# Kernel tuning notes

Hardware: AMD Instinct MI355X
Metric: run time of the kernel (lower is better)

Reference implementation:

```python
import jax, jax.numpy as jnp
import numpy as np

DIM = 4096
HEAD_DIM = 512
ROPE_DIM = 64
NOPE_DIM = HEAD_DIM - ROPE_DIM  # 448
RATIO = 4
COFF = 2  # overlap since ratio == 4
EPS = 1e-6
NEG = -1e30
COMPRESS_ROPE_THETA = 40000.0


def _hadamard(n):
    H = np.array([[1.0]], dtype=np.float32)
    while H.shape[0] < n:
        H = np.block([[H, H], [H, -H]])
    return (H / np.sqrt(n)).astype(np.float32)

H_MAT = jnp.asarray(_hadamard(HEAD_DIM))  # [512, 512], orthonormal Hadamard


def setup_inputs() -> dict:
    key = jax.random.key(0)
    ks = jax.random.split(key, 5)
    b, s = 4, 4096
    x = jax.random.normal(ks[0], (b, s, DIM), dtype=jnp.float32)
    W_kv = jax.random.normal(ks[1], (COFF * HEAD_DIM, DIM), dtype=jnp.float32) * 0.02
    W_gate = jax.random.normal(ks[2], (COFF * HEAD_DIM, DIM), dtype=jnp.float32) * 0.02
    ape = jax.random.normal(ks[3], (RATIO, COFF * HEAD_DIM), dtype=jnp.float32) * 0.02
    norm_w = jnp.ones((HEAD_DIM,), dtype=jnp.float32)
    # rotary table over compressed-block positions
    nb = s // RATIO
    inv_freq = 1.0 / (COMPRESS_ROPE_THETA ** (jnp.arange(0, ROPE_DIM, 2, dtype=jnp.float32) / ROPE_DIM))
    ang = jnp.arange(nb, dtype=jnp.float32)[:, None] * inv_freq[None, :]  # [nb, 32]
    freqs_cis = jnp.stack([jnp.cos(ang), jnp.sin(ang)], axis=-1)  # [nb, 32, 2]
    return {"x": x, "W_kv": W_kv, "W_gate": W_gate, "ape": ape,
            "norm_w": norm_w, "freqs_cis": freqs_cis, "start_pos": 0}


def _overlap_transform(t, fill):
    # t: [b, nb, RATIO, 2*d] -> [b, nb, 2*RATIO, d]
    b, nb, r, dd = t.shape
    d = dd // 2
    prev_first = jnp.concatenate(
        [jnp.full((b, 1, r, d), fill, t.dtype), t[:, :-1, :, :d]], axis=1)
    return jnp.concatenate([prev_first, t[..., d:]], axis=2)


def reference(x, W_kv, W_gate, ape, norm_w, freqs_cis, start_pos):
    b, s, _ = x.shape
    nb = s // RATIO
    # block-wise projections with absolute-within-block positional bias
    kv = jnp.einsum('bsd,od->bso', x, W_kv).reshape(b, nb, RATIO, COFF * HEAD_DIM) + ape
    score = jnp.einsum('bsd,od->bso', x, W_gate).reshape(b, nb, RATIO, COFF * HEAD_DIM)
    # overlap with previous block: [b, nb, 2*RATIO, HEAD_DIM]
    kv_w = _overlap_transform(kv, 0.0)
    sc_w = _overlap_transform(score, NEG)
    # channelwise softmax-gated pooling over the 2*RATIO window
    w = jax.nn.softmax(sc_w, axis=2)
    pooled = jnp.sum(w * kv_w, axis=2)  # [b, nb, HEAD_DIM]
    # RMSNorm
    var = jnp.mean(jnp.square(pooled), axis=-1, keepdims=True)
    pooled = norm_w * (pooled * jax.lax.rsqrt(var + EPS))
    # rotary on the rope slice
    nope, rope = pooled[..., :NOPE_DIM], pooled[..., NOPE_DIM:]
    rp = rope.reshape(b, nb, ROPE_DIM // 2, 2)
    xr, xi = rp[..., 0], rp[..., 1]
    fr, fi = freqs_cis[None, :, :, 0], freqs_cis[None, :, :, 1]
    rot = jnp.stack([xr * fr - xi * fi, xr * fi + xi * fr], axis=-1).reshape(b, nb, ROPE_DIM)
    out = jnp.concatenate([nope, rot], axis=-1)  # [b, nb, HEAD_DIM]
    # Hadamard rotation (rotate_activation)
    out = out @ H_MAT
    return out
```

## Files before the change

### kernel.cpp

```cpp
#include <hip/hip_runtime.h>
#include <hip/hip_bf16.h>
#include <stdint.h>

#define M_ROWS 16384
#define N_COLS 2048
#define K_DIM  4096
#define NEGV   -1e30f

typedef __bf16 bfv8 __attribute__((ext_vector_type(8)));
typedef float  f32x4 __attribute__((ext_vector_type(4)));
typedef unsigned short u16;

static __device__ __forceinline__ u16 f32_to_bf16_rne(float f) {
  union { float f; unsigned int u; } v; v.f = f;
  unsigned int u = v.u;
  u += 0x7fffu + ((u >> 16) & 1u);
  return (u16)(u >> 16);
}

static __device__ __forceinline__ float b2f(u16 b) {
  union { unsigned int u; float f; } v; v.u = ((unsigned int)b) << 16;
  return v.f;
}

__global__ __launch_bounds__(256) void k_cvt(const float* __restrict__ x,
                                             const float* __restrict__ wkv,
                                             const float* __restrict__ wg,
                                             u16* __restrict__ dst) {
  long i = (long)blockIdx.x * blockDim.x + threadIdx.x;
  long base = i * 8;
  const float* src;
  if (base < 67108864L) {
    src = x + base;
  } else {
    long wi = base - 67108864L;
    src = (wi < 4194304L) ? (wkv + wi) : (wg + (wi - 4194304L));
  }
  float4 a = *(const float4*)(src);
  float4 b = *(const float4*)(src + 4);
  union { u16 s[8]; uint4 v; } o;
  o.s[0] = f32_to_bf16_rne(a.x); o.s[1] = f32_to_bf16_rne(a.y);
  o.s[2] = f32_to_bf16_rne(a.z); o.s[3] = f32_to_bf16_rne(a.w);
  o.s[4] = f32_to_bf16_rne(b.x); o.s[5] = f32_to_bf16_rne(b.y);
  o.s[6] = f32_to_bf16_rne(b.z); o.s[7] = f32_to_bf16_rne(b.w);
  *(uint4*)(dst + base) = o.v;
}

#define GLD16(g, l) __builtin_amdgcn_global_load_lds( \
    (const __attribute__((address_space(1))) unsigned int*)(g), \
    (__attribute__((address_space(3))) unsigned int*)(l), 16, 0, 0)

#define SB0 __builtin_amdgcn_sched_barrier(0)
#define BAR __builtin_amdgcn_s_barrier()
#define VM4 asm volatile("s_waitcnt vmcnt(4)" ::: "memory")

__global__ __launch_bounds__(512, 2) void k_gemm(const u16* __restrict__ A,
                                                 const u16* __restrict__ B,
                                                 u16* __restrict__ C) {
  __shared__ u16 lds[65536];

  const int tid  = threadIdx.x;
  const int wid  = tid >> 6;
  const int lane = tid & 63;
  const int wr = wid >> 2, wc = wid & 3;
  const int fr = lane & 15, fq = lane >> 4;

  int o = blockIdx.x;
  int swz = (o & 7) * 64 + (o >> 3);
  const int bm = swz >> 3, bn = swz & 7;
  const int gm0 = bm << 8, gn0 = bn << 8;

  int aoff[8], boff[4];
#pragma unroll
  for (int mi = 0; mi < 8; ++mi) {
    int row = (wr << 7) + (mi << 4) + fr;
    int Gp = (((row & 1) << 2) | fq) ^ ((row >> 1) & 7);
    aoff[mi] = (row >> 1) * 64 + Gp * 8;
  }
#pragma unroll
  for (int ni = 0; ni < 4; ++ni) {
    int row = (wc << 6) + (ni << 4) + fr;
    int Gp = (((row & 1) << 2) | fq) ^ ((row >> 1) & 7);
    boff[ni] = (row >> 1) * 64 + Gp * 8;
  }

  const int s0 = tid, s1 = 512 + tid;
  const int l0 = s0 >> 3, G0 = (s0 & 7) ^ (l0 & 7);
  const int r0 = 2 * l0 + (G0 >> 2), g0 = (G0 & 3) << 3;
  const int l1 = s1 >> 3, G1 = (s1 & 7) ^ (l1 & 7);
  const int r1 = 2 * l1 + (G1 >> 2), g1 = (G1 & 3) << 3;
  const u16* pA0 = A + ((size_t)(gm0 + r0) << 12) + g0;
  const u16* pA1 = A + ((size_t)(gm0 + r1) << 12) + g1;
  const u16* pB0 = B + ((size_t)(gn0 + r0) << 12) + g0;
  const u16* pB1 = B + ((size_t)(gn0 + r1) << 12) + g1;
  const int du0 = wid << 9;
  const int du1 = 4096 + (wid << 9);

#define STAGE_A(Q, KK, KTN) do { \
  GLD16(pA0 + (KTN) + (KK) * 32, &lds[(Q) * 16384 + (KK) * 8192 + du0]); \
  GLD16(pA1 + (KTN) + (KK) * 32, &lds[(Q) * 16384 + (KK) * 8192 + du1]); } while (0)
#define STAGE_B(Q, KK, KTN) do { \
  GLD16(pB0 + (KTN) + (KK) * 32, &lds[32768 + (Q) * 16384 + (KK) * 8192 + du0]); \
  GLD16(pB1 + (KTN) + (KK) * 32, &lds[32768 + (Q) * 16384 + (KK) * 8192 + du1]); } while (0)
#define LDA(P, KK, MI) (*(const bfv8*)&lds[(P) * 16384 + (KK) * 8192 + aoff[MI]])
#define LDB(P, KK, NI) (*(const bfv8*)&lds[32768 + (P) * 16384 + (KK) * 8192 + boff[NI]])
#define MF(AV, BV, MI, NI) acc[MI][NI] = __builtin_amdgcn_mfma_f32_16x16x32_bf16(AV, BV, acc[MI][NI], 0, 0, 0)
#define MF4(AV, MI) do { MF(AV, b0, MI, 0); MF(AV, b1, MI, 1); MF(AV, b2, MI, 2); MF(AV, b3, MI, 3); } while (0)

  f32x4 acc[8][4];
#pragma unroll
  for (int i = 0; i < 8; ++i)
#pragma unroll
    for (int j = 0; j < 4; ++j) acc[i][j] = (f32x4){0.f, 0.f, 0.f, 0.f};

  STAGE_A(0, 0, 0); STAGE_B(0, 0, 0); STAGE_A(0, 1, 0); STAGE_B(0, 1, 0);
  SB0; VM4; BAR; SB0;

  bfv8 a0, a1, a2, a3, a4, a5, a6, a7, b0, b1, b2, b3;

#define KTILE(P, Q, KTN) do { \
  a0 = LDA(P, 0, 0); a1 = LDA(P, 0, 1); a2 = LDA(P, 0, 2); a3 = LDA(P, 0, 3); \
  b0 = LDB(P, 0, 0); b1 = LDB(P, 0, 1); b2 = LDB(P, 0, 2); b3 = LDB(P, 0, 3); \
  STAGE_A(Q, 0, KTN); \
  SB0; BAR; SB0; \
  __builtin_amdgcn_s_setprio(1); \
  MF4(a0, 0); MF4(a1, 1); MF4(a2, 2); MF4(a3, 3); \
  __builtin_amdgcn_s_setprio(0); SB0; \
  a4 = LDA(P, 0, 4); a5 = LDA(P, 0, 5); a6 = LDA(P, 0, 6); a7 = LDA(P, 0, 7); \
  STAGE_B(Q, 0, KTN); \
  SB0; VM4; BAR; SB0; \
  __builtin_amdgcn_s_setprio(1); \
  MF4(a4, 4); MF4(a5, 5); MF4(a6, 6); MF4(a7, 7); \
  __builtin_amdgcn_s_setprio(0); SB0; \
  a0 = LDA(P, 1, 0); a1 = LDA(P, 1, 1); a2 = LDA(P, 1, 2); a3 = LDA(P, 1, 3); \
  b0 = LDB(P, 1, 0); b1 = LDB(P, 1, 1); b2 = LDB(P, 1, 2); b3 = LDB(P, 1, 3); \
  STAGE_A(Q, 1, KTN); \
  SB0; BAR; SB0; \
  __builtin_amdgcn_s_setprio(1); \
  MF4(a0, 0); MF4(a1, 1); MF4(a2, 2); MF4(a3, 3); \
  __builtin_amdgcn_s_setprio(0); SB0; \
  a4 = LDA(P, 1, 4); a5 = LDA(P, 1, 5); a6 = LDA(P, 1, 6); a7 = LDA(P, 1, 7); \
  STAGE_B(Q, 1, KTN); \
  SB0; VM4; BAR; SB0; \
  __builtin_amdgcn_s_setprio(1); \
  MF4(a4, 4); MF4(a5, 5); MF4(a6, 6); MF4(a7, 7); \
  __builtin_amdgcn_s_setprio(0); SB0; \
} while (0)

  for (int i = 0; i < 32; ++i) {
    const int kt1 = (2 * i + 1) << 6;
    const int kt2 = (i == 31) ? 0 : (2 * i + 2) << 6;
    KTILE(0, 1, kt1);
    KTILE(1, 0, kt2);
  }

#pragma unroll
  for (int mi = 0; mi < 8; ++mi) {
    int row = gm0 + (wr << 7) + (mi << 4) + (fq << 2);
#pragma unroll
    for (int ni = 0; ni < 4; ++ni) {
      int col = gn0 + (wc << 6) + (ni << 4) + fr;
#pragma unroll
      for (int j = 0; j < 4; ++j)
        C[(size_t)(row + j) * N_COLS + col] = f32_to_bf16_rne(acc[mi][ni][j]);
    }
  }
#undef KTILE
#undef STAGE_A
#undef STAGE_B
#undef LDA
#undef LDB
#undef MF
#undef MF4
}

__global__ __launch_bounds__(256) void k_pool(const u16* __restrict__ kvsc,
                                              const float* __restrict__ ape,
                                              const float* __restrict__ norm_w,
                                              const float* __restrict__ freqs,
                                              float* __restrict__ out) {
  __shared__ float sm[512];
  __shared__ float red[8];
  const int tid = threadIdx.x;
  const int bid = blockIdx.x;
  const int b = bid >> 10, ib = bid & 1023;

  float ss = 0.f;
#pragma unroll
  for (int cc = 0; cc < 2; ++cc) {
    int c = tid + (cc << 8);
    float kvv[8], scv[8];
    if (ib > 0) {
      size_t mb = ((size_t)b * 4096 + (size_t)(ib - 1) * 4);
#pragma unroll
      for (int p = 0; p < 4; ++p) {
        size_t ro = (mb + p) * N_COLS;
        kvv[p] = b2f(kvsc[ro + c]) + ape[p * 1024 + c];
        scv[p] = b2f(kvsc[ro + 1024 + c]);
      }
    } else {
#pragma unroll
      for (int p = 0; p < 4; ++p) { kvv[p] = 0.f; scv[p] = NEGV; }
    }
    size_t mb2 = ((size_t)b * 4096 + (size_t)ib * 4);
#pragma unroll
    for (int r = 0; r < 4; ++r) {
      size_t ro = (mb2 + r) * N_COLS;
      kvv[4 + r] = b2f(kvsc[ro + 512 + c]) + ape[r * 1024 + 512 + c];
      scv[4 + r] = b2f(kvsc[ro + 1024 + 512 + c]);
    }
    float mx = scv[0];
#pragma unroll
    for (int p = 1; p < 8; ++p) mx = fmaxf(mx, scv[p]);
    float se = 0.f, ac = 0.f;
#pragma unroll
    for (int p = 0; p < 8; ++p) {
      float e = __expf(scv[p] - mx);
      se += e; ac += e * kvv[p];
    }
    float pooled = ac / se;
    sm[c] = pooled;
    ss += pooled * pooled;
  }
#pragma unroll
  for (int m = 1; m < 64; m <<= 1) ss += __shfl_xor(ss, m, 64);
  if ((tid & 63) == 0) red[tid >> 6] = ss;
  __syncthreads();
  float sumsq = red[0] + red[1] + red[2] + red[3];
  float scale = rsqrtf(sumsq * (1.f / 512.f) + 1e-6f);
  sm[tid]       = sm[tid]       * scale * norm_w[tid];
  sm[tid + 256] = sm[tid + 256] * scale * norm_w[tid + 256];
  __syncthreads();
  if (tid < 32) {
    int j = tid;
    float xr = sm[448 + 2 * j], xi = sm[449 + 2 * j];
    float fr = freqs[((size_t)ib * 32 + j) * 2];
    float fi = freqs[((size_t)ib * 32 + j) * 2 + 1];
    sm[448 + 2 * j] = xr * fr - xi * fi;
    sm[449 + 2 * j] = xr * fi + xi * fr;
  }
  __syncthreads();
#pragma unroll
  for (int k = 0; k < 9; ++k) {
    int low = tid & ((1 << k) - 1);
    int i0 = ((tid >> k) << (k + 1)) | low;
    int i1 = i0 | (1 << k);
    float a = sm[i0], bb = sm[i1];
    sm[i0] = a + bb; sm[i1] = a - bb;
    __syncthreads();
  }
  const float OSC = 0.044194173824159216f;
  size_t ob = (size_t)bid * 512;
  out[ob + tid]       = sm[tid] * OSC;
  out[ob + tid + 256] = sm[tid + 256] * OSC;
}

extern "C" void kernel_launch(void* const* d_in, const int* in_sizes, int n_in,
                              void* d_out, int out_size, void* d_ws, size_t ws_size,
                              hipStream_t stream) {
  const float* x      = (const float*)d_in[0];
  const float* W_kv   = (const float*)d_in[1];
  const float* W_gate = (const float*)d_in[2];
  const float* ape    = (const float*)d_in[3];
  const float* norm_w = (const float*)d_in[4];
  const float* freqs  = (const float*)d_in[5];
  float* out = (float*)d_out;

  char* ws = (char*)d_ws;
  u16* xb   = (u16*)ws;
  u16* wb   = (u16*)(ws + 134217728L);
  u16* kvsc = (u16*)(ws + 134217728L + 16777216L);

  hipLaunchKernelGGL(k_cvt, dim3(36864), dim3(256), 0, stream, x, W_kv, W_gate, xb);
  hipLaunchKernelGGL(k_gemm, dim3(512), dim3(512), 0, stream, xb, wb, kvsc);
  hipLaunchKernelGGL(k_pool, dim3(4096), dim3(256), 0, stream, kvsc, ape, norm_w, freqs, out);
}
```

Baseline: 313.4 us.

## Load B fragments directly from global into registers, bypassing LDS

The B operand of the GEMM is no longer staged through shared memory. Each wave now loads its B MFMA fragments straight from global memory into registers, double-buffered in two register sets (u/v), while A keeps its LDS pipeline. This halves LDS use per block and removes the LDS reads for B. In exchange, B is fetched redundantly by the waves that share a column, the loads are uncoalesced 16-byte row reads, the vmcnt waits had to be retuned, and register pressure rises.

```diff
diff --git a/kernel.cpp b/kernel.cpp
--- a/kernel.cpp
+++ b/kernel.cpp
@@ -52,12 +52,13 @@
 
 #define SB0 __builtin_amdgcn_sched_barrier(0)
 #define BAR __builtin_amdgcn_s_barrier()
-#define VM4 asm volatile("s_waitcnt vmcnt(4)" ::: "memory")
+#define VM6 asm volatile("s_waitcnt vmcnt(6)" ::: "memory")
+#define VM0 asm volatile("s_waitcnt vmcnt(0)" ::: "memory")
 
 __global__ __launch_bounds__(512, 2) void k_gemm(const u16* __restrict__ A,
                                                  const u16* __restrict__ B,
                                                  u16* __restrict__ C) {
-  __shared__ u16 lds[65536];
+  __shared__ u16 lds[32768];
 
   const int tid  = threadIdx.x;
   const int wid  = tid >> 6;
@@ -70,19 +71,18 @@
   const int bm = swz >> 3, bn = swz & 7;
   const int gm0 = bm << 8, gn0 = bn << 8;
 
-  int aoff[8], boff[4];
+  int aoff[8];
 #pragma unroll
   for (int mi = 0; mi < 8; ++mi) {
     int row = (wr << 7) + (mi << 4) + fr;
     int Gp = (((row & 1) << 2) | fq) ^ ((row >> 1) & 7);
     aoff[mi] = (row >> 1) * 64 + Gp * 8;
   }
-#pragma unroll
-  for (int ni = 0; ni < 4; ++ni) {
-    int row = (wc << 6) + (ni << 4) + fr;
-    int Gp = (((row & 1) << 2) | fq) ^ ((row >> 1) & 7);
-    boff[ni] = (row >> 1) * 64 + Gp * 8;
-  }
+
+  const u16* pBf0 = B + ((size_t)(gn0 + (wc << 6) +  0 + fr) << 12) + (fq << 3);
+  const u16* pBf1 = B + ((size_t)(gn0 + (wc << 6) + 16 + fr) << 12) + (fq << 3);
+  const u16* pBf2 = B + ((size_t)(gn0 + (wc << 6) + 32 + fr) << 12) + (fq << 3);
+  const u16* pBf3 = B + ((size_t)(gn0 + (wc << 6) + 48 + fr) << 12) + (fq << 3);
 
   const int s0 = tid, s1 = 512 + tid;
   const int l0 = s0 >> 3, G0 = (s0 & 7) ^ (l0 & 7);
@@ -91,21 +91,22 @@
   const int r1 = 2 * l1 + (G1 >> 2), g1 = (G1 & 3) << 3;
   const u16* pA0 = A + ((size_t)(gm0 + r0) << 12) + g0;
   const u16* pA1 = A + ((size_t)(gm0 + r1) << 12) + g1;
-  const u16* pB0 = B + ((size_t)(gn0 + r0) << 12) + g0;
-  const u16* pB1 = B + ((size_t)(gn0 + r1) << 12) + g1;
   const int du0 = wid << 9;
   const int du1 = 4096 + (wid << 9);
 
 #define STAGE_A(Q, KK, KTN) do { \
   GLD16(pA0 + (KTN) + (KK) * 32, &lds[(Q) * 16384 + (KK) * 8192 + du0]); \
   GLD16(pA1 + (KTN) + (KK) * 32, &lds[(Q) * 16384 + (KK) * 8192 + du1]); } while (0)
-#define STAGE_B(Q, KK, KTN) do { \
-  GLD16(pB0 + (KTN) + (KK) * 32, &lds[32768 + (Q) * 16384 + (KK) * 8192 + du0]); \
-  GLD16(pB1 + (KTN) + (KK) * 32, &lds[32768 + (Q) * 16384 + (KK) * 8192 + du1]); } while (0)
 #define LDA(P, KK, MI) (*(const bfv8*)&lds[(P) * 16384 + (KK) * 8192 + aoff[MI]])
-#define LDB(P, KK, NI) (*(const bfv8*)&lds[32768 + (P) * 16384 + (KK) * 8192 + boff[NI]])
+#define BLOADU(KT) do { \
+  u0 = *(const bfv8*)(pBf0 + (KT)); u1 = *(const bfv8*)(pBf1 + (KT)); \
+  u2 = *(const bfv8*)(pBf2 + (KT)); u3 = *(const bfv8*)(pBf3 + (KT)); } while (0)
+#define BLOADV(KT) do { \
+  v0 = *(const bfv8*)(pBf0 + (KT)); v1 = *(const bfv8*)(pBf1 + (KT)); \
+  v2 = *(const bfv8*)(pBf2 + (KT)); v3 = *(const bfv8*)(pBf3 + (KT)); } while (0)
 #define MF(AV, BV, MI, NI) acc[MI][NI] = __builtin_amdgcn_mfma_f32_16x16x32_bf16(AV, BV, acc[MI][NI], 0, 0, 0)
-#define MF4(AV, MI) do { MF(AV, b0, MI, 0); MF(AV, b1, MI, 1); MF(AV, b2, MI, 2); MF(AV, b3, MI, 3); } while (0)
+#define MF4U(AV, MI) do { MF(AV, u0, MI, 0); MF(AV, u1, MI, 1); MF(AV, u2, MI, 2); MF(AV, u3, MI, 3); } while (0)
+#define MF4V(AV, MI) do { MF(AV, v0, MI, 0); MF(AV, v1, MI, 1); MF(AV, v2, MI, 2); MF(AV, v3, MI, 3); } while (0)
 
   f32x4 acc[8][4];
 #pragma unroll
@@ -113,45 +114,46 @@
 #pragma unroll
     for (int j = 0; j < 4; ++j) acc[i][j] = (f32x4){0.f, 0.f, 0.f, 0.f};
 
-  STAGE_A(0, 0, 0); STAGE_B(0, 0, 0); STAGE_A(0, 1, 0); STAGE_B(0, 1, 0);
-  SB0; VM4; BAR; SB0;
-
-  bfv8 a0, a1, a2, a3, a4, a5, a6, a7, b0, b1, b2, b3;
-
-#define KTILE(P, Q, KTN) do { \
+  bfv8 a0, a1, a2, a3, a4, a5, a6, a7;
+  bfv8 u0, u1, u2, u3, v0, v1, v2, v3;
+
+  BLOADU(0);
+  STAGE_A(0, 0, 0); STAGE_A(0, 1, 0);
+  SB0; VM0; BAR; SB0;
+
+#define KTILE(P, Q, KT1, KT2) do { \
   a0 = LDA(P, 0, 0); a1 = LDA(P, 0, 1); a2 = LDA(P, 0, 2); a3 = LDA(P, 0, 3); \
-  b0 = LDB(P, 0, 0); b1 = LDB(P, 0, 1); b2 = LDB(P, 0, 2); b3 = LDB(P, 0, 3); \
-  STAGE_A(Q, 0, KTN); \
+  BLOADV((KT1) + 32); \
+  STAGE_A(Q, 0, KT2); \
   SB0; BAR; SB0; \
   __builtin_amdgcn_s_setprio(1); \
-  MF4(a0, 0); MF4(a1, 1); MF4(a2, 2); MF4(a3, 3); \
+  MF4U(a0, 0); MF4U(a1, 1); MF4U(a2, 2); MF4U(a3, 3); \
   __builtin_amdgcn_s_setprio(0); SB0; \
   a4 = LDA(P, 0, 4); a5 = LDA(P, 0, 5); a6 = LDA(P, 0, 6); a7 = LDA(P, 0, 7); \
-  STAGE_B(Q, 0, KTN); \
-  SB0; VM4; BAR; SB0; \
-  __builtin_amdgcn_s_setprio(1); \
-  MF4(a4, 4); MF4(a5, 5); MF4(a6, 6); MF4(a7, 7); \
+  SB0; VM6; BAR; SB0; \
+  __builtin_amdgcn_s_setprio(1); \
+  MF4U(a4, 4); MF4U(a5, 5); MF4U(a6, 6); MF4U(a7, 7); \
   __builtin_amdgcn_s_setprio(0); SB0; \
   a0 = LDA(P, 1, 0); a1 = LDA(P, 1, 1); a2 = LDA(P, 1, 2); a3 = LDA(P, 1, 3); \
-  b0 = LDB(P, 1, 0); b1 = LDB(P, 1, 1); b2 = LDB(P, 1, 2); b3 = LDB(P, 1, 3); \
-  STAGE_A(Q, 1, KTN); \
+  BLOADU(KT2); \
+  STAGE_A(Q, 1, KT2); \
   SB0; BAR; SB0; \
   __builtin_amdgcn_s_setprio(1); \
-  MF4(a0, 0); MF4(a1, 1); MF4(a2, 2); MF4(a3, 3); \
+  MF4V(a0, 0); MF4V(a1, 1); MF4V(a2, 2); MF4V(a3, 3); \
   __builtin_amdgcn_s_setprio(0); SB0; \
   a4 = LDA(P, 1, 4); a5 = LDA(P, 1, 5); a6 = LDA(P, 1, 6); a7 = LDA(P, 1, 7); \
-  STAGE_B(Q, 1, KTN); \
-  SB0; VM4; BAR; SB0; \
-  __builtin_amdgcn_s_setprio(1); \
-  MF4(a4, 4); MF4(a5, 5); MF4(a6, 6); MF4(a7, 7); \
+  SB0; VM6; BAR; SB0; \
+  __builtin_amdgcn_s_setprio(1); \
+  MF4V(a4, 4); MF4V(a5, 5); MF4V(a6, 6); MF4V(a7, 7); \
   __builtin_amdgcn_s_setprio(0); SB0; \
 } while (0)
 
   for (int i = 0; i < 32; ++i) {
-    const int kt1 = (2 * i + 1) << 6;
-    const int kt2 = (i == 31) ? 0 : (2 * i + 2) << 6;
-    KTILE(0, 1, kt1);
-    KTILE(1, 0, kt2);
+    const int ktA = (2 * i) << 6;
+    const int ktB = (2 * i + 1) << 6;
+    const int ktC = (i == 31) ? 0 : (2 * i + 2) << 6;
+    KTILE(0, 1, ktA, ktB);
+    KTILE(1, 0, ktB, ktC);
   }
 
 #pragma unroll
@@ -167,11 +169,12 @@
   }
 #undef KTILE
 #undef STAGE_A
-#undef STAGE_B
 #undef LDA
-#undef LDB
+#undef BLOADU
+#undef BLOADV
 #undef MF
-#undef MF4
+#undef MF4U
+#undef MF4V
 }
 
 __global__ __launch_bounds__(256) void k_pool(const u16* __restrict__ kvsc,
```

Result: slower. 493.5 us (+57.5%).
